# Kernel optimization log

Measured on AMD Instinct MI355X. Metric: run time of the kernel, lower is better.

## Reference

```python
import jax, jax.numpy as jnp
import numpy as np

B, S, D, H, K, MLP, ZD = 8, 2048, 1024, 16, 256, 4096, 1024
DH = D // H
EPS = 1e-6


def setup_inputs() -> dict:
    key = jax.random.key(0)
    ks = jax.random.split(key, 32)
    g = lambda i, shape, scale=0.02: jax.random.normal(ks[i], shape, dtype=jnp.float32) * scale
    inp = {
        "x": jax.random.normal(ks[0], (B, S, D), dtype=jnp.float32),
        "z": jax.random.normal(ks[1], (B, ZD), dtype=jnp.float32),
        # attention projections
        "wq": g(2, (D, D)), "bq": jnp.zeros((D,), jnp.float32),
        "wk": g(3, (D, D)), "bk": jnp.zeros((D,), jnp.float32),
        "wv": g(4, (D, D)), "bv": jnp.zeros((D,), jnp.float32),
        # Linformer sequence projections (kernel over seq dim)
        "Ew": g(5, (S, K)), "Eb": jnp.zeros((K,), jnp.float32),
        "Fw": g(6, (S, K)), "Fb": jnp.zeros((K,), jnp.float32),
        "wo": g(7, (D, D)), "bo": jnp.zeros((D,), jnp.float32),
        # adaLN 1
        "h1w": g(8, (ZD, D)), "h1b": jnp.zeros((D,), jnp.float32),
        "g1w": g(9, (D, D)), "g1b": jnp.ones((D,), jnp.float32),
        "be1w": g(10, (D, D)), "be1b": jnp.zeros((D,), jnp.float32),
        # adaLN 2
        "h2w": g(11, (ZD, D)), "h2b": jnp.zeros((D,), jnp.float32),
        "g2w": g(12, (D, D)), "g2b": jnp.ones((D,), jnp.float32),
        "be2w": g(13, (D, D)), "be2b": jnp.zeros((D,), jnp.float32),
        # MLP
        "m1w": g(14, (D, MLP)), "m1b": jnp.zeros((MLP,), jnp.float32),
        "m2w": g(15, (MLP, D)), "m2b": jnp.zeros((D,), jnp.float32),
    }
    return inp


def _adaln(x, z, hw, hb, gw, gb, bw, bb):
    # moments over feature axis, normalize, then conditioned scale/shift
    mean = jnp.mean(x, axis=2, keepdims=True)
    var = jnp.var(x, axis=2, keepdims=True)
    xn = (x - mean) * jax.lax.rsqrt(var + EPS)
    h = jax.nn.silu(z @ hw + hb)              # [B, D]
    scale = h @ gw + gb                        # [B, D]
    offset = h @ bw + bb                       # [B, D]
    return xn * scale[:, None, :] + offset[:, None, :]


def _linformer_attn(x, wq, bq, wk, bk, wv, bv, Ew, Eb, Fw, Fb, wo, bo):
    q = (x @ wq + bq).reshape(B, S, H, DH).transpose(0, 2, 1, 3)  # [B,H,S,dh]
    k = (x @ wk + bk).reshape(B, S, H, DH).transpose(0, 2, 1, 3)
    v = (x @ wv + bv).reshape(B, S, H, DH).transpose(0, 2, 1, 3)
    # project seq dim S -> K (Dense applied to [B,H,dh,S]); bias adds on K axis
    k = jnp.einsum('bhsd,sk->bhkd', k, Ew) + Eb[None, None, :, None]  # [B,H,K,dh]
    v = jnp.einsum('bhsd,sk->bhkd', v, Fw) + Fb[None, None, :, None]
    scores = jnp.einsum('bhsd,bhkd->bhsk', q, k) / jnp.sqrt(jnp.float32(DH))
    attn = jax.nn.softmax(scores, axis=-1)
    out = jnp.einsum('bhsk,bhkd->bhsd', attn, v)  # [B,H,S,dh]
    out = out.transpose(0, 2, 1, 3).reshape(B, S, D)
    return out @ wo + bo


def reference(x, z, wq, bq, wk, bk, wv, bv, Ew, Eb, Fw, Fb, wo, bo,
              h1w, h1b, g1w, g1b, be1w, be1b,
              h2w, h2b, g2w, g2b, be2w, be2b,
              m1w, m1b, m2w, m2b):
    x1 = _adaln(x, z, h1w, h1b, g1w, g1b, be1w, be1b)
    attn_out = x + _linformer_attn(x1, wq, bq, wk, bk, wv, bv, Ew, Eb, Fw, Fb, wo, bo)
    x2 = _adaln(attn_out, z, h2w, h2b, g2w, g2b, be2w, be2b)
    hmid = jax.nn.gelu(x2 @ m1w + m1b, approximate=False)
    mlp_out = hmid @ m2w + m2b
    return mlp_out + attn_out
```

## Files before the change

### kernel.cpp

```cpp
#include <hip/hip_runtime.h>
#include <math.h>

#define AS1 __attribute__((address_space(1)))
#define AS3 __attribute__((address_space(3)))

typedef short bf16x8 __attribute__((ext_vector_type(8)));
typedef short s16x4  __attribute__((ext_vector_type(4)));
typedef float f32x4  __attribute__((ext_vector_type(4)));

#define MFMA(a,b,c) __builtin_amdgcn_mfma_f32_16x16x32_bf16((a),(b),(c),0,0,0)

__device__ __forceinline__ short f2bf(float f) {
  union { float f; unsigned u; } v; v.f = f;
  unsigned r = v.u + 0x7FFFu + ((v.u >> 16) & 1u);
  return (short)(r >> 16);
}

__device__ __forceinline__ void gload16(const void* g, void* l) {
  __builtin_amdgcn_global_load_lds((const AS1 void*)g, (AS3 void*)l, 16, 0, 0);
}

__global__ __launch_bounds__(256) void k_transpose_cvt(
    const float* __restrict__ in, short* __restrict__ out, int R, int C) {
  __shared__ float t[64][65];
  int c0 = blockIdx.x * 64, r0 = blockIdx.y * 64;
  int tx = threadIdx.x & 63, ty = threadIdx.x >> 6;
  for (int r = ty; r < 64; r += 4)
    t[r][tx] = in[(size_t)(r0 + r) * C + c0 + tx];
  __syncthreads();
  for (int c = ty; c < 64; c += 4)
    out[(size_t)(c0 + c) * R + r0 + tx] = f2bf(t[tx][c]);
}

__global__ __launch_bounds__(256) void k_cond_h(
    const float* __restrict__ z,
    const float* __restrict__ h1w, const float* __restrict__ h1b,
    const float* __restrict__ h2w, const float* __restrict__ h2b,
    float* __restrict__ hbuf) {
  int dl = threadIdx.x & 63, kq = threadIdx.x >> 6;
  int d = blockIdx.x * 64 + dl;
  int b = blockIdx.y, sel = blockIdx.z;
  const float* W = (sel ? h2w : h1w) + (size_t)(kq * 256) * 1024 + d;
  const float* zr = z + b * 1024 + kq * 256;
  float acc = 0.f;
  for (int i = 0; i < 256; ++i) acc = fmaf(zr[i], W[(size_t)i * 1024], acc);
  __shared__ float red[256];
  red[threadIdx.x] = acc;
  __syncthreads();
  if (kq == 0) {
    float v = red[dl] + red[dl + 64] + red[dl + 128] + red[dl + 192];
    v += (sel ? h2b : h1b)[d];
    hbuf[(size_t)(sel * 8 + b) * 1024 + d] = v / (1.f + expf(-v));
  }
}

__global__ __launch_bounds__(256) void k_cond_so(
    const float* __restrict__ hbuf,
    const float* __restrict__ g1w, const float* __restrict__ g1b,
    const float* __restrict__ be1w, const float* __restrict__ be1b,
    const float* __restrict__ g2w, const float* __restrict__ g2b,
    const float* __restrict__ be2w, const float* __restrict__ be2b,
    float* __restrict__ so) {
  int dl = threadIdx.x & 63, kq = threadIdx.x >> 6;
  int d = blockIdx.x * 64 + dl;
  int b = blockIdx.y, sel = blockIdx.z;
  const float* W = sel == 0 ? g1w : sel == 1 ? be1w : sel == 2 ? g2w : be2w;
  const float* bias = sel == 0 ? g1b : sel == 1 ? be1b : sel == 2 ? g2b : be2b;
  const float* hr = hbuf + (size_t)((sel >> 1) * 8 + b) * 1024 + kq * 256;
  const float* Wp = W + (size_t)(kq * 256) * 1024 + d;
  float acc = 0.f;
  for (int i = 0; i < 256; ++i) acc = fmaf(hr[i], Wp[(size_t)i * 1024], acc);
  __shared__ float red[256];
  red[threadIdx.x] = acc;
  __syncthreads();
  if (kq == 0) {
    float v = red[dl] + red[dl + 64] + red[dl + 128] + red[dl + 192] + bias[d];
    so[(size_t)(sel * 8 + b) * 1024 + d] = v;
  }
}

__global__ __launch_bounds__(256) void k_adaln(
    const float* __restrict__ xin, const float* __restrict__ so,
    int which, short* __restrict__ xout) {
  int row = blockIdx.x;
  int b = row >> 11;
  const float4* xr = (const float4*)(xin + (size_t)row * 1024);
  float4 v = xr[threadIdx.x];
  float s = v.x + v.y + v.z + v.w;
  float sq = v.x * v.x + v.y * v.y + v.z * v.z + v.w * v.w;
#pragma unroll
  for (int o = 32; o >= 1; o >>= 1) {
    s += __shfl_xor(s, o, 64);
    sq += __shfl_xor(sq, o, 64);
  }
  __shared__ float red[8];
  int wid = threadIdx.x >> 6;
  if ((threadIdx.x & 63) == 0) { red[wid] = s; red[4 + wid] = sq; }
  __syncthreads();
  s = red[0] + red[1] + red[2] + red[3];
  sq = red[4] + red[5] + red[6] + red[7];
  float mean = s * (1.f / 1024.f);
  float var = sq * (1.f / 1024.f) - mean * mean;
  float rstd = rsqrtf(var + 1e-6f);
  const float4* scp = (const float4*)(so + (size_t)(which * 2) * 8192 + b * 1024);
  const float4* ofp = (const float4*)(so + (size_t)(which * 2 + 1) * 8192 + b * 1024);
  float4 sc = scp[threadIdx.x], of = ofp[threadIdx.x];
  s16x4 o;
  o[0] = f2bf((v.x - mean) * rstd * sc.x + of.x);
  o[1] = f2bf((v.y - mean) * rstd * sc.y + of.y);
  o[2] = f2bf((v.z - mean) * rstd * sc.z + of.z);
  o[3] = f2bf((v.w - mean) * rstd * sc.w + of.w);
  *(s16x4*)(xout + (size_t)row * 1024 + threadIdx.x * 4) = o;
}

enum { EPI_QKV = 0, EPI_KP = 1, EPI_VPT = 2, EPI_RESID = 3, EPI_GELU = 4 };

template <int EPI>
__global__ __launch_bounds__(256) void k_gemm(
    const short* __restrict__ A, long sA, int lda,
    const short* __restrict__ BT, long sBT, int ldbt,
    int Kd,
    short* __restrict__ o0, short* __restrict__ o1, short* __restrict__ o2,
    const float* __restrict__ b0, const float* __restrict__ b1,
    const float* __restrict__ b2,
    const float* __restrict__ resid, float* __restrict__ fo, long sC) {
  int t = threadIdx.x, lane = t & 63, wid = t >> 6;
  int wr = wid >> 1, wc = wid & 1;
  int n0 = blockIdx.x * 128, m0 = blockIdx.y * 128, bz = blockIdx.z;
  const short* Ab = A + (long)bz * sA;
  const short* Bb = BT + (long)bz * sBT;
  __shared__ short lds[8192];
  const short* gA = Ab + (long)(m0 + (t >> 2)) * lda + (t & 3) * 8;
  const short* gB = Bb + (long)(n0 + (t >> 2)) * ldbt + (t & 3) * 8;
  char* lA = (char*)lds + wid * 1024;
  char* lB = (char*)lds + 8192 + wid * 1024;
  const long a64 = (long)64 * lda, b64s = (long)64 * ldbt;
  f32x4 acc[4][4];
#pragma unroll
  for (int m = 0; m < 4; ++m)
#pragma unroll
    for (int n = 0; n < 4; ++n) acc[m][n] = (f32x4){0.f, 0.f, 0.f, 0.f};

  int rsel = lane & 15, koff = (lane >> 4) * 16;
  for (int k = 0; k < Kd; k += 32) {
    gload16(gA, lA);
    gload16(gA + a64, lA + 4096);
    gload16(gB, lB);
    gload16(gB + b64s, lB + 4096);
    gA += 32; gB += 32;
    __syncthreads();
    bf16x8 af[4], bfr[4];
#pragma unroll
    for (int m = 0; m < 4; ++m)
      af[m] = *(const bf16x8*)((const char*)lds + (wr * 64 + m * 16 + rsel) * 64 + koff);
#pragma unroll
    for (int n = 0; n < 4; ++n)
      bfr[n] = *(const bf16x8*)((const char*)lds + 8192 + (wc * 64 + n * 16 + rsel) * 64 + koff);
#pragma unroll
    for (int m = 0; m < 4; ++m)
#pragma unroll
      for (int n = 0; n < 4; ++n)
        acc[m][n] = MFMA(af[m], bfr[n], acc[m][n]);
    __syncthreads();
  }

  int cl = lane & 15, rh = lane >> 4;
#pragma unroll
  for (int m = 0; m < 4; ++m) {
    int rgb = m0 + wr * 64 + m * 16 + rh * 4;
#pragma unroll
    for (int n = 0; n < 4; ++n) {
      int cg = n0 + wc * 64 + n * 16 + cl;
      f32x4 a = acc[m][n];
      if constexpr (EPI == EPI_KP) {
        short* dst = o0 + (long)bz * sC;
#pragma unroll
        for (int r = 0; r < 4; ++r)
          dst[(size_t)(rgb + r) * 1024 + cg] = f2bf(a[r] + b0[rgb + r]);
      } else if constexpr (EPI == EPI_VPT) {
        short* dst = o0 + (long)bz * sC;
        s16x4 pk;
#pragma unroll
        for (int r = 0; r < 4; ++r) pk[r] = f2bf(a[r] + b0[rgb + r]);
        *(s16x4*)(dst + (long)cg * 256 + rgb) = pk;
      }
    }
  }
}

template <int EPI>
__global__ __launch_bounds__(512, 2) void k_gemm256(
    const short* __restrict__ A, int lda,
    const short* __restrict__ BT, int ldbt,
    int Kd, int ntN,
    short* __restrict__ o0, short* __restrict__ o1, short* __restrict__ o2,
    const float* __restrict__ bi0, const float* __restrict__ bi1,
    const float* __restrict__ bi2,
    const float* __restrict__ resid, float* __restrict__ fo) {
  __shared__ __align__(16) char lds[131072];
  int t = threadIdx.x, lane = t & 63, wid = t >> 6;
  int wr = wid >> 2, wc = wid & 3;
  int l15 = lane & 15;
  int lko = ((lane >> 4) * 16) ^ (((l15 >> 2) & 1) << 5);

  int nwg = gridDim.x, o = blockIdx.x;
  int swz = (o & 7) * (nwg >> 3) + (o >> 3);
  int mt = swz / ntN, nt = swz - mt * ntN;
  int m0 = mt * 256, n0 = nt * 256;

  int p0 = t * 16;
  int sl = p0 ^ (((p0 >> 9) & 1) << 5);
  int srow = sl >> 7, scol = sl & 127;
  const char* A8 = (const char*)A;
  const char* B8 = (const char*)BT;
  size_t ldab = (size_t)lda * 2, ldbb = (size_t)ldbt * 2;
  size_t aoff = (size_t)(m0 + srow) * ldab + scol;
  size_t boff = (size_t)(n0 + srow) * ldbb + scol;
  char* ldsw = (char*)lds + wid * 1024;

  auto stage = [&](int H, int kt, int buf) {
    char* d = ldsw + buf * 65536 + H * 16384;
    if (H < 2) {
      const char* s = A8 + aoff + (size_t)(H * 128) * ldab + (size_t)kt * 128;
      gload16(s, d);
      gload16(s + 64 * ldab, d + 8192);
    } else {
      const char* s = B8 + boff + (size_t)((H - 2) * 128) * ldbb + (size_t)kt * 128;
      gload16(s, d);
      gload16(s + 64 * ldbb, d + 8192);
    }
  };

  const char* LA = (const char*)lds + wr * 16384 + l15 * 128 + lko;
  const char* LB = (const char*)lds + 32768 + (wc >> 1) * 16384 + (wc & 1) * 8192 +
                   l15 * 128 + lko;

  f32x4 acc[8][4];
#pragma unroll
  for (int m = 0; m < 8; ++m)
#pragma unroll
    for (int n = 0; n < 4; ++n) acc[m][n] = (f32x4){0.f, 0.f, 0.f, 0.f};

  bf16x8 af[4][2], Bv0[2][2], Bv1[2][2];

#define RDA(buf, mi, ks) (*(const bf16x8*)(LA + (buf) * 65536 + (mi) * 2048 + (ks) * 64))
#define RDB(buf, ni, ks) (*(const bf16x8*)(LB + (buf) * 65536 + (ni) * 2048 + (ks) * 64))
#define PH_TAIL(MB, NB, BARR)                                         \
  __builtin_amdgcn_s_barrier();                                       \
  asm volatile("s_waitcnt lgkmcnt(0)" ::: "memory");                  \
  __builtin_amdgcn_sched_barrier(0);                                  \
  __builtin_amdgcn_s_setprio(1);                                      \
  _Pragma("unroll") for (int mi = 0; mi < 4; ++mi)                    \
  _Pragma("unroll") for (int ni = 0; ni < 2; ++ni)                    \
  _Pragma("unroll") for (int ks = 0; ks < 2; ++ks)                    \
      acc[(MB) + mi][(NB) + ni] =                                     \
          MFMA(af[mi][ks], BARR[ni][ks], acc[(MB) + mi][(NB) + ni]);  \
  __builtin_amdgcn_s_setprio(0);                                      \
  __builtin_amdgcn_s_barrier();

  int NT = Kd >> 6, NI = NT >> 1, msk = NT - 1;

  stage(0, 0, 0); stage(1, 0, 0); stage(2, 0, 0); stage(3, 0, 0);
  stage(0, 1, 1);
  asm volatile("s_waitcnt vmcnt(2)" ::: "memory");
  __builtin_amdgcn_s_barrier();

  auto half = [&](int bf, int tkA, int bufA, int tkB, int bufB) {
#pragma unroll
    for (int mi = 0; mi < 4; ++mi)
#pragma unroll
      for (int ks = 0; ks < 2; ++ks) af[mi][ks] = RDA(bf, mi, ks);
#pragma unroll
    for (int ni = 0; ni < 2; ++ni)
#pragma unroll
      for (int ks = 0; ks < 2; ++ks) Bv0[ni][ks] = RDB(bf, ni, ks);
    stage(1, tkA, bufA);
    PH_TAIL(0, 0, Bv0)
#pragma unroll
    for (int ni = 0; ni < 2; ++ni)
#pragma unroll
      for (int ks = 0; ks < 2; ++ks) Bv1[ni][ks] = RDB(bf, ni + 2, ks);
    stage(2, tkA, bufA);
    PH_TAIL(0, 2, Bv1)
#pragma unroll
    for (int mi = 0; mi < 4; ++mi)
#pragma unroll
      for (int ks = 0; ks < 2; ++ks) af[mi][ks] = RDA(bf, mi + 4, ks);
    stage(3, tkA, bufA);
    PH_TAIL(4, 2, Bv1)
    stage(0, tkB, bufB);
    asm volatile("s_waitcnt vmcnt(2)" ::: "memory");
    PH_TAIL(4, 0, Bv0)
  };

  for (int i = 0; i < NI; ++i) {
    int T1k = 2 * i + 1, T2k = (2 * i + 2) & msk, T3k = (2 * i + 3) & msk;
    half(0, T1k, 1, T2k, 0);
    half(1, T2k, 0, T3k, 1);
  }

  int cl = l15, rh = lane >> 4;
#pragma unroll
  for (int m = 0; m < 8; ++m) {
    int rgb = m0 + wr * 128 + m * 16 + rh * 4;
#pragma unroll
    for (int n = 0; n < 4; ++n) {
      int cg = n0 + wc * 64 + n * 16 + cl;
      f32x4 a = acc[m][n];
      if constexpr (EPI == EPI_QKV) {
        int sec = n0 >> 10;
        int cloc = cg & 1023;
        float bias = (sec == 0 ? bi0 : sec == 1 ? bi1 : bi2)[cloc];
        if (sec == 0) {
#pragma unroll
          for (int r = 0; r < 4; ++r)
            o0[(size_t)(rgb + r) * 1024 + cloc] = f2bf(a[r] + bias);
        } else {
          short* dst = (sec == 1) ? o1 : o2;
          int bb = rgb >> 11, slc = rgb & 2047;
          s16x4 pk;
#pragma unroll
          for (int r = 0; r < 4; ++r) pk[r] = f2bf(a[r] + bias);
          *(s16x4*)(dst + ((long)bb * 1024 + cloc) * 2048 + slc) = pk;
        }
      } else if constexpr (EPI == EPI_RESID) {
        float bias = bi0[cg];
#pragma unroll
        for (int r = 0; r < 4; ++r) {
          size_t idx = (size_t)(rgb + r) * 1024 + cg;
          fo[idx] = a[r] + bias + resid[idx];
        }
      } else if constexpr (EPI == EPI_GELU) {
        float bias = bi0[cg];
#pragma unroll
        for (int r = 0; r < 4; ++r) {
          float xv = a[r] + bias;
          float g = 0.5f * xv * (1.f + erff(xv * 0.70710678118654752f));
          o0[(size_t)(rgb + r) * 4096 + cg] = f2bf(g);
        }
      }
    }
  }
#undef RDA
#undef RDB
#undef PH_TAIL
}

__global__ __launch_bounds__(256) void k_attn(
    const short* __restrict__ q, const short* __restrict__ kp,
    const short* __restrict__ vpt, short* __restrict__ oh) {
  int lane = threadIdx.x & 63, wid = threadIdx.x >> 6;
  int h = blockIdx.y, b = blockIdx.z;
  int s0 = blockIdx.x * 64 + wid * 16;
  int cl = lane & 15, rh = lane >> 4;
  __shared__ short plds[4][16][264];

  const short* qbase = q + ((size_t)(b * 2048 + s0 + cl)) * 1024 + h * 64 + rh * 8;
  bf16x8 qa0 = *(const bf16x8*)qbase;
  bf16x8 qa1 = *(const bf16x8*)(qbase + 32);

  f32x4 sc[16];
  const short* kb = kp + ((size_t)(b * 256 + cl)) * 1024 + h * 64 + rh * 8;
#pragma unroll
  for (int n = 0; n < 16; ++n) {
    const short* kn = kb + (size_t)(n * 16) * 1024;
    f32x4 a = (f32x4){0.f, 0.f, 0.f, 0.f};
    a = MFMA(qa0, *(const bf16x8*)kn, a);
    a = MFMA(qa1, *(const bf16x8*)(kn + 32), a);
    sc[n] = a * 0.125f;
  }

  float mx[4] = {-1e30f, -1e30f, -1e30f, -1e30f};
#pragma unroll
  for (int n = 0; n < 16; ++n)
#pragma unroll
    for (int r = 0; r < 4; ++r) mx[r] = fmaxf(mx[r], sc[n][r]);
#pragma unroll
  for (int o = 1; o < 16; o <<= 1)
#pragma unroll
    for (int r = 0; r < 4; ++r) mx[r] = fmaxf(mx[r], __shfl_xor(mx[r], o, 64));

  float sm[4] = {0.f, 0.f, 0.f, 0.f};
#pragma unroll
  for (int n = 0; n < 16; ++n)
#pragma unroll
    for (int r = 0; r < 4; ++r) {
      float e = expf(sc[n][r] - mx[r]);
      sc[n][r] = e;
      sm[r] += e;
    }
#pragma unroll
  for (int o = 1; o < 16; o <<= 1)
#pragma unroll
    for (int r = 0; r < 4; ++r) sm[r] += __shfl_xor(sm[r], o, 64);
  float inv[4];
#pragma unroll
  for (int r = 0; r < 4; ++r) inv[r] = 1.f / sm[r];

#pragma unroll
  for (int n = 0; n < 16; ++n)
#pragma unroll
    for (int r = 0; r < 4; ++r)
      plds[wid][rh * 4 + r][n * 16 + cl] = f2bf(sc[n][r] * inv[r]);
  asm volatile("s_waitcnt lgkmcnt(0)" ::: "memory");

  bf16x8 pa[8];
#pragma unroll
  for (int c = 0; c < 8; ++c)
    pa[c] = *(const bf16x8*)&plds[wid][cl][c * 32 + rh * 8];

  const short* vb = vpt + ((size_t)(b * 1024 + h * 64 + cl)) * 256 + rh * 8;
  short* ob = oh + ((size_t)(b * 2048 + s0 + rh * 4)) * 1024 + h * 64 + cl;
#pragma unroll
  for (int n = 0; n < 4; ++n) {
    f32x4 a = (f32x4){0.f, 0.f, 0.f, 0.f};
    const short* vn = vb + (size_t)(n * 16) * 256;
#pragma unroll
    for (int c = 0; c < 8; ++c)
      a = MFMA(pa[c], *(const bf16x8*)(vn + c * 32), a);
#pragma unroll
    for (int r = 0; r < 4; ++r)
      ob[(size_t)r * 1024 + n * 16] = f2bf(a[r]);
  }
}

extern "C" void kernel_launch(void* const* d_in, const int* in_sizes, int n_in,
                              void* d_out, int out_size, void* d_ws, size_t ws_size,
                              hipStream_t stream) {
  (void)in_sizes; (void)n_in; (void)out_size; (void)ws_size;
  const float* x    = (const float*)d_in[0];
  const float* z    = (const float*)d_in[1];
  const float* wq   = (const float*)d_in[2];
  const float* bq   = (const float*)d_in[3];
  const float* wk   = (const float*)d_in[4];
  const float* bk   = (const float*)d_in[5];
  const float* wv   = (const float*)d_in[6];
  const float* bv   = (const float*)d_in[7];
  const float* Ew   = (const float*)d_in[8];
  const float* Eb   = (const float*)d_in[9];
  const float* Fw   = (const float*)d_in[10];
  const float* Fb   = (const float*)d_in[11];
  const float* wo   = (const float*)d_in[12];
  const float* bo   = (const float*)d_in[13];
  const float* h1w  = (const float*)d_in[14];
  const float* h1b  = (const float*)d_in[15];
  const float* g1w  = (const float*)d_in[16];
  const float* g1b  = (const float*)d_in[17];
  const float* be1w = (const float*)d_in[18];
  const float* be1b = (const float*)d_in[19];
  const float* h2w  = (const float*)d_in[20];
  const float* h2b  = (const float*)d_in[21];
  const float* g2w  = (const float*)d_in[22];
  const float* g2b  = (const float*)d_in[23];
  const float* be2w = (const float*)d_in[24];
  const float* be2b = (const float*)d_in[25];
  const float* m1w  = (const float*)d_in[26];
  const float* m1b  = (const float*)d_in[27];
  const float* m2w  = (const float*)d_in[28];
  const float* m2b  = (const float*)d_in[29];
  float* out = (float*)d_out;

  char* ws = (char*)d_ws;
  size_t off = 0;
  auto alloc = [&](size_t bytes) {
    char* p = ws + off;
    off += (bytes + 255) & ~(size_t)255;
    return p;
  };
  short* x1  = (short*)alloc((size_t)32 << 20);
  short* qb  = (short*)alloc((size_t)32 << 20);
  short* kT  = (short*)alloc((size_t)32 << 20);
  short* vT  = (short*)alloc((size_t)32 << 20);
  short* ah  = (short*)alloc((size_t)32 << 20);
  short* kpj = (short*)alloc((size_t)4 << 20);
  short* vpt = (short*)alloc((size_t)4 << 20);
  short* wqkvT = (short*)alloc((size_t)3072 * 1024 * 2);
  short* woT   = (short*)alloc((size_t)1024 * 1024 * 2);
  short* m1T   = (short*)alloc((size_t)4096 * 1024 * 2);
  short* m2T   = (short*)alloc((size_t)1024 * 4096 * 2);
  short* EwT   = (short*)alloc((size_t)256 * 2048 * 2);
  short* FwT   = (short*)alloc((size_t)256 * 2048 * 2);
  float* hbuf  = (float*)alloc((size_t)2 * 8 * 1024 * 4);
  float* sobuf = (float*)alloc((size_t)4 * 8 * 1024 * 4);
  float* aout = (float*)kT;
  short* x2   = ah;
  short* hmid = x1;

  dim3 blk(256);
  k_transpose_cvt<<<dim3(16, 16), blk, 0, stream>>>(wq, wqkvT, 1024, 1024);
  k_transpose_cvt<<<dim3(16, 16), blk, 0, stream>>>(wk, wqkvT + 1024 * 1024, 1024, 1024);
  k_transpose_cvt<<<dim3(16, 16), blk, 0, stream>>>(wv, wqkvT + 2 * 1024 * 1024, 1024, 1024);
  k_transpose_cvt<<<dim3(16, 16), blk, 0, stream>>>(wo, woT, 1024, 1024);
  k_transpose_cvt<<<dim3(64, 16), blk, 0, stream>>>(m1w, m1T, 1024, 4096);
  k_transpose_cvt<<<dim3(16, 64), blk, 0, stream>>>(m2w, m2T, 4096, 1024);
  k_transpose_cvt<<<dim3(4, 32), blk, 0, stream>>>(Ew, EwT, 2048, 256);
  k_transpose_cvt<<<dim3(4, 32), blk, 0, stream>>>(Fw, FwT, 2048, 256);
  k_cond_h<<<dim3(16, 8, 2), blk, 0, stream>>>(z, h1w, h1b, h2w, h2b, hbuf);
  k_cond_so<<<dim3(16, 8, 4), blk, 0, stream>>>(hbuf, g1w, g1b, be1w, be1b,
                                                g2w, g2b, be2w, be2b, sobuf);
  k_adaln<<<dim3(16384), blk, 0, stream>>>(x, sobuf, 0, x1);
  k_gemm256<EPI_QKV><<<dim3(768), dim3(512), 0, stream>>>(
      x1, 1024, wqkvT, 1024, 1024, 12,
      qb, kT, vT, bq, bk, bv, nullptr, nullptr);
  k_gemm<EPI_KP><<<dim3(8, 2, 8), blk, 0, stream>>>(
      EwT, 0, 2048, kT, (long)1024 * 2048, 2048, 2048,
      kpj, nullptr, nullptr, Eb, nullptr, nullptr, nullptr, nullptr, 262144);
  k_gemm<EPI_VPT><<<dim3(8, 2, 8), blk, 0, stream>>>(
      FwT, 0, 2048, vT, (long)1024 * 2048, 2048, 2048,
      vpt, nullptr, nullptr, Fb, nullptr, nullptr, nullptr, nullptr, 262144);
  k_attn<<<dim3(32, 16, 8), blk, 0, stream>>>(qb, kpj, vpt, ah);
  k_gemm256<EPI_RESID><<<dim3(256), dim3(512), 0, stream>>>(
      ah, 1024, woT, 1024, 1024, 4,
      nullptr, nullptr, nullptr, bo, nullptr, nullptr, x, aout);
  k_adaln<<<dim3(16384), blk, 0, stream>>>(aout, sobuf, 1, x2);
  for (int c = 0; c < 2; ++c) {
    const short* x2c = x2 + (size_t)c * 8192 * 1024;
    const float* aoc = aout + (size_t)c * 8192 * 1024;
    float* outc = out + (size_t)c * 8192 * 1024;
    k_gemm256<EPI_GELU><<<dim3(512), dim3(512), 0, stream>>>(
        x2c, 1024, m1T, 1024, 1024, 16,
        hmid, nullptr, nullptr, m1b, nullptr, nullptr, nullptr, nullptr);
    k_gemm256<EPI_RESID><<<dim3(128), dim3(512), 0, stream>>>(
        hmid, 4096, m2T, 4096, 4096, 4,
        nullptr, nullptr, nullptr, m2b, nullptr, nullptr, aoc, outc);
  }
}
```

Measured before the change: 1.116 ms.

## Switch GEMM LDS swizzle to row-based XOR and drop explicit lgkmcnt wait

Replaces the old LDS layout swizzle in the 256x256 GEMM with a row-indexed XOR swizzle across 16-byte chunks. The per-lane fragment offsets for the two k-halves are reordered to match, which is meant to cut LDS bank conflicts on the ds_read path. The staging addresses are precomputed per half so the stage lambda needs less address arithmetic. It also removes the explicit lgkmcnt(0) wait and sched_barrier before the MFMA block, letting the compiler schedule waits itself, at some risk to ordering and overlap.

```diff
diff --git a/kernel.cpp b/kernel.cpp
--- a/kernel.cpp
+++ b/kernel.cpp
@@ -201,7 +201,9 @@
   int t = threadIdx.x, lane = t & 63, wid = t >> 6;
   int wr = wid >> 2, wc = wid & 3;
   int l15 = lane & 15;
-  int lko = ((lane >> 4) * 16) ^ (((l15 >> 2) & 1) << 5);
+  int q16x = ((lane >> 4) * 16) ^ ((l15 & 3) << 4);
+  int kf64 = ((l15 >> 2) & 1) << 6;
+  int k0o = kf64, k1o = 64 - kf64;
 
   int nwg = gridDim.x, o = blockIdx.x;
   int swz = (o & 7) * (nwg >> 3) + (o >> 3);
@@ -209,31 +211,27 @@
   int m0 = mt * 256, n0 = nt * 256;
 
   int p0 = t * 16;
-  int sl = p0 ^ (((p0 >> 9) & 1) << 5);
-  int srow = sl >> 7, scol = sl & 127;
-  const char* A8 = (const char*)A;
-  const char* B8 = (const char*)BT;
+  int srow = p0 >> 7;
+  int scol = (p0 & 127) ^ ((srow & 7) << 4);
   size_t ldab = (size_t)lda * 2, ldbb = (size_t)ldbt * 2;
-  size_t aoff = (size_t)(m0 + srow) * ldab + scol;
-  size_t boff = (size_t)(n0 + srow) * ldbb + scol;
+  const char* sA0 = (const char*)A + (size_t)(m0 + srow) * ldab + scol;
+  const char* sA1 = sA0 + 128 * ldab;
+  const char* sB0 = (const char*)BT + (size_t)(n0 + srow) * ldbb + scol;
+  const char* sB1 = sB0 + 128 * ldbb;
   char* ldsw = (char*)lds + wid * 1024;
 
   auto stage = [&](int H, int kt, int buf) {
+    const char* s = (H == 0 ? sA0 : H == 1 ? sA1 : H == 2 ? sB0 : sB1) +
+                    ((size_t)kt << 7);
+    size_t ld64 = (H < 2 ? ldab : ldbb) << 6;
     char* d = ldsw + buf * 65536 + H * 16384;
-    if (H < 2) {
-      const char* s = A8 + aoff + (size_t)(H * 128) * ldab + (size_t)kt * 128;
-      gload16(s, d);
-      gload16(s + 64 * ldab, d + 8192);
-    } else {
-      const char* s = B8 + boff + (size_t)((H - 2) * 128) * ldbb + (size_t)kt * 128;
-      gload16(s, d);
-      gload16(s + 64 * ldbb, d + 8192);
-    }
+    gload16(s, d);
+    gload16(s + ld64, d + 8192);
   };
 
-  const char* LA = (const char*)lds + wr * 16384 + l15 * 128 + lko;
+  const char* LA = (const char*)lds + wr * 16384 + l15 * 128 + q16x;
   const char* LB = (const char*)lds + 32768 + (wc >> 1) * 16384 + (wc & 1) * 8192 +
-                   l15 * 128 + lko;
+                   l15 * 128 + q16x;
 
   f32x4 acc[8][4];
 #pragma unroll
@@ -243,12 +241,12 @@
 
   bf16x8 af[4][2], Bv0[2][2], Bv1[2][2];
 
-#define RDA(buf, mi, ks) (*(const bf16x8*)(LA + (buf) * 65536 + (mi) * 2048 + (ks) * 64))
-#define RDB(buf, ni, ks) (*(const bf16x8*)(LB + (buf) * 65536 + (ni) * 2048 + (ks) * 64))
+#define RDA(buf, mi, ks) \
+  (*(const bf16x8*)(LA + (buf) * 65536 + (mi) * 2048 + ((ks) ? k1o : k0o)))
+#define RDB(buf, ni, ks) \
+  (*(const bf16x8*)(LB + (buf) * 65536 + (ni) * 2048 + ((ks) ? k1o : k0o)))
 #define PH_TAIL(MB, NB, BARR)                                         \
   __builtin_amdgcn_s_barrier();                                       \
-  asm volatile("s_waitcnt lgkmcnt(0)" ::: "memory");                  \
-  __builtin_amdgcn_sched_barrier(0);                                  \
   __builtin_amdgcn_s_setprio(1);                                      \
   _Pragma("unroll") for (int mi = 0; mi < 4; ++mi)                    \
   _Pragma("unroll") for (int ni = 0; ni < 2; ++ni)                    \
```

Result: no change. 1.095 ms (-1.9%).
